# Kernel optimization log

Measured on AMD Instinct MI355X. Metric: run time of the kernel, lower is better.

## Reference

```python
import jax, jax.numpy as jnp
import numpy as np

H = 512      # hidden_size
V = 50257    # output_size (vocab)
M = 200      # memory_size
B = 64       # batch


def setup_inputs() -> dict:
    key = jax.random.key(0)
    ks = jax.random.split(key, 24)
    s = 1.0 / np.sqrt(H)
    f32 = jnp.float32
    return {
        "rmn_hidden": jax.random.normal(ks[0], (1, B, H), f32),
        "cell": jax.random.normal(ks[1], (1, B, H), f32),
        "context": jax.random.normal(ks[2], (1, B, H), f32),
        # embedding tables
        "emb": jax.random.normal(ks[3], (V, H), f32) * 0.02,
        "m_emb": jax.random.normal(ks[4], (V, H), f32) * 0.02,
        "c_emb": jax.random.normal(ks[5], (V, H), f32) * 0.02,
        # LSTMCell(2H -> H), torch gate order i, f, g, o
        "lstm_W_ih": jax.random.normal(ks[6], (4 * H, 2 * H), f32) * s,
        "lstm_W_hh": jax.random.normal(ks[7], (4 * H, H), f32) * s,
        "lstm_b_ih": jax.random.normal(ks[8], (4 * H,), f32) * s,
        "lstm_b_hh": jax.random.normal(ks[9], (4 * H,), f32) * s,
        # GRUCell(H -> H), torch gate order r, z, n
        "gru_W_ih": jax.random.normal(ks[10], (3 * H, H), f32) * s,
        "gru_W_hh": jax.random.normal(ks[11], (3 * H, H), f32) * s,
        "gru_b_ih": jax.random.normal(ks[12], (3 * H,), f32) * s,
        "gru_b_hh": jax.random.normal(ks[13], (3 * H,), f32) * s,
        # mb_attn_linear(M -> M)
        "attn_W": jax.random.normal(ks[14], (M, M), f32) * (1.0 / np.sqrt(M)),
        "attn_b": jax.random.normal(ks[15], (M,), f32) * (1.0 / np.sqrt(M)),
        # out Linear(2H -> V)
        "out_W": jax.random.normal(ks[16], (V, 2 * H), f32) * (1.0 / np.sqrt(2 * H)),
        "out_b": jax.random.normal(ks[17], (V,), f32) * (1.0 / np.sqrt(2 * H)),
        # int inputs
        "input_ids": jax.random.randint(ks[18], (1, B), 0, V, jnp.int32),
        "memory_tensor": jax.random.randint(ks[19], (M, B), 0, V, jnp.int32),
        "batch_size": B,
        "memory_size": M,
    }


def reference(rmn_hidden, cell, context, emb, m_emb, c_emb,
              lstm_W_ih, lstm_W_hh, lstm_b_ih, lstm_b_hh,
              gru_W_ih, gru_W_hh, gru_b_ih, gru_b_hh,
              attn_W, attn_b, out_W, out_b,
              input_ids, memory_tensor, batch_size, memory_size):
    sig = jax.nn.sigmoid
    h = rmn_hidden.shape[-1]
    # embedding + relu, concat with context along feature dim
    x = jax.nn.relu(emb[input_ids])                       # (1, B, H)
    ctx = context.reshape(1, batch_size, h)               # (1, B, H)
    xc = jnp.concatenate([x, ctx], axis=2)[0]             # (B, 2H)
    h0, c0 = rmn_hidden[0], cell[0]                       # (B, H)
    # LSTMCell
    gates = xc @ lstm_W_ih.T + lstm_b_ih + h0 @ lstm_W_hh.T + lstm_b_hh
    i, f, g, o = jnp.split(gates, 4, axis=-1)
    c1 = sig(f) * c0 + sig(i) * jnp.tanh(g)
    h1 = sig(o) * jnp.tanh(c1)                            # lstm_hidden (B, H)
    # memory attention
    in_mem = m_emb[memory_tensor]                         # (M, B, H)
    out_mem = c_emb[memory_tensor]                        # (M, B, H)
    attn = jnp.einsum('mbh,bh->bm', in_mem, h1)           # (B, M)
    attn = attn @ attn_W.T + attn_b
    # NOTE: original applies nn.LogSoftmax here (not Softmax) -- faithful.
    attn_dist = jax.nn.log_softmax(attn, axis=-1)         # (B, M)
    memory_context = jnp.einsum('mbh,bm->bh', out_mem, attn_dist)  # (B, H)
    # GRUCell(memory_context, h1)
    gi = memory_context @ gru_W_ih.T + gru_b_ih
    gh = h1 @ gru_W_hh.T + gru_b_hh
    gi_r, gi_z, gi_n = jnp.split(gi, 3, axis=-1)
    gh_r, gh_z, gh_n = jnp.split(gh, 3, axis=-1)
    r = sig(gi_r + gh_r)
    z = sig(gi_z + gh_z)
    n = jnp.tanh(gi_n + r * gh_n)
    mb = (1.0 - z) * n + z * h1                           # (B, H)
    # output projection + log-softmax
    mbc = jnp.concatenate([mb[None], ctx], axis=2)[0]     # (B, 2H)
    output = jax.nn.log_softmax(mbc @ out_W.T + out_b, axis=-1)  # (B, V)
    return (output, h1, c1[None])
```

## Files before the change

kernel.cpp:

```cpp
#include <hip/hip_runtime.h>
#include <math.h>

#define B 64
#define H 512
#define V 50257
#define M 200
#define H2 1024
#define H3 1536
#define H4 2048
#define NB 786

typedef short short8 __attribute__((ext_vector_type(8)));
typedef float f32x4 __attribute__((ext_vector_type(4)));

__device__ __forceinline__ float sigf(float x) { return 1.f / (1.f + expf(-x)); }

__device__ __forceinline__ short bf16c(float f) {
  unsigned u = __builtin_bit_cast(unsigned, f);
  unsigned r = u + 0x7fffu + ((u >> 16) & 1u);
  return (short)(r >> 16);
}

__global__ __launch_bounds__(256) void k_build_A(
    const float* __restrict__ emb, const float* __restrict__ ctx,
    const float* __restrict__ h0, const int* __restrict__ ids,
    short* __restrict__ A) {
  int k = blockIdx.x * 256 + threadIdx.x;
  int b = blockIdx.y;
  float v;
  if (k < 512) {
    v = emb[(size_t)ids[b] * H + k];
    v = v > 0.f ? v : 0.f;
  } else if (k < 1024) {
    v = ctx[b * H + (k - 512)];
  } else {
    v = h0[b * H + (k - 1024)];
  }
  A[b * H3 + k] = bf16c(v);
}

__global__ __launch_bounds__(256) void k_lstm_gates_mfma(
    const short* __restrict__ A, const float* __restrict__ W_ih,
    const float* __restrict__ W_hh, const float* __restrict__ b_ih,
    const float* __restrict__ b_hh, float* __restrict__ gates) {
  __shared__ float sred[3][64][16];
  const int tid = threadIdx.x;
  const int lane = tid & 63, wid = tid >> 6;
  const int col = lane & 15, g = lane >> 4;
  const int j = blockIdx.x * 16 + col;
  const int kbase = wid * 384;

  f32x4 acc[4];
  #pragma unroll
  for (int t = 0; t < 4; ++t) acc[t] = (f32x4)(0.f);

  #pragma unroll 2
  for (int it = 0; it < 12; ++it) {
    int k0 = kbase + it * 32;
    const float* wp;
    if (k0 < 1024) wp = W_ih + (size_t)j * H2 + k0 + g * 8;
    else           wp = W_hh + (size_t)j * H + (k0 - 1024) + g * 8;
    float4 wa = *(const float4*)wp;
    float4 wb = *(const float4*)(wp + 4);
    short8 bf;
    bf[0] = bf16c(wa.x); bf[1] = bf16c(wa.y); bf[2] = bf16c(wa.z); bf[3] = bf16c(wa.w);
    bf[4] = bf16c(wb.x); bf[5] = bf16c(wb.y); bf[6] = bf16c(wb.z); bf[7] = bf16c(wb.w);
    #pragma unroll
    for (int t = 0; t < 4; ++t) {
      short8 af = *(const short8*)(A + (size_t)(col + t * 16) * H3 + k0 + g * 8);
      acc[t] = __builtin_amdgcn_mfma_f32_16x16x32_bf16(af, bf, acc[t], 0, 0, 0);
    }
  }

  if (wid) {
    #pragma unroll
    for (int t = 0; t < 4; ++t)
      #pragma unroll
      for (int r = 0; r < 4; ++r) sred[wid - 1][lane][t * 4 + r] = acc[t][r];
  }
  __syncthreads();
  if (wid == 0) {
    float bias = b_ih[j] + b_hh[j];
    #pragma unroll
    for (int t = 0; t < 4; ++t)
      #pragma unroll
      for (int r = 0; r < 4; ++r) {
        float s = acc[t][r] + sred[0][lane][t * 4 + r] + sred[1][lane][t * 4 + r] +
                  sred[2][lane][t * 4 + r];
        int brow = t * 16 + g * 4 + r;
        gates[brow * H4 + j] = s + bias;
      }
  }
}

__global__ __launch_bounds__(256) void k_lstm_cell(
    const float* __restrict__ gates, const float* __restrict__ c0,
    float* __restrict__ h1, float* __restrict__ c1, short* __restrict__ h1bf) {
  int idx = blockIdx.x * 256 + threadIdx.x;
  int b = idx >> 9, h = idx & 511;
  const float* g = gates + b * H4;
  float gi = g[h], gf = g[H + h], gg = g[2 * H + h], go = g[3 * H + h];
  float c = sigf(gf) * c0[idx] + sigf(gi) * tanhf(gg);
  c1[idx] = c;
  float hv = sigf(go) * tanhf(c);
  h1[idx] = hv;
  h1bf[idx] = bf16c(hv);
}

__global__ __launch_bounds__(256) void k_attn_scores(
    const float* __restrict__ m_emb, const int* __restrict__ mt,
    const float* __restrict__ h1, float* __restrict__ attn) {
  int wave = (blockIdx.x * 256 + threadIdx.x) >> 6;
  int lane = threadIdx.x & 63;
  int m = wave >> 6, b = wave & 63;
  int row = mt[m * B + b];
  const float4* e = (const float4*)(m_emb + (size_t)row * H);
  const float4* hv = (const float4*)(h1 + b * H);
  float4 a0 = e[lane], a1 = e[64 + lane];
  float4 b0 = hv[lane], b1 = hv[64 + lane];
  float acc = a0.x * b0.x + a0.y * b0.y + a0.z * b0.z + a0.w * b0.w +
              a1.x * b1.x + a1.y * b1.y + a1.z * b1.z + a1.w * b1.w;
  for (int off = 32; off > 0; off >>= 1) acc += __shfl_down(acc, off);
  if (lane == 0) attn[b * M + m] = acc;
}

__global__ __launch_bounds__(256) void k_attn_lin_lsm(
    const float* __restrict__ attn, const float* __restrict__ attn_W,
    const float* __restrict__ attn_b, float* __restrict__ attn_d) {
  __shared__ float arow[M];
  __shared__ float vals[256];
  __shared__ float red[256];
  int b = blockIdx.x, tid = threadIdx.x;
  if (tid < M) arow[tid] = attn[b * M + tid];
  __syncthreads();
  float v = -1e30f;
  if (tid < M) {
    const float* w = attn_W + tid * M;
    float a0 = attn_b[tid], a1 = 0.f;
    for (int m = 0; m < M; m += 2) {
      a0 = fmaf(arow[m], w[m], a0);
      a1 = fmaf(arow[m + 1], w[m + 1], a1);
    }
    v = a0 + a1;
  }
  vals[tid] = v;
  red[tid] = v;
  __syncthreads();
  for (int off = 128; off > 0; off >>= 1) {
    if (tid < off) red[tid] = fmaxf(red[tid], red[tid + off]);
    __syncthreads();
  }
  float mx = red[0];
  __syncthreads();
  red[tid] = (tid < M) ? expf(vals[tid] - mx) : 0.f;
  __syncthreads();
  for (int off = 128; off > 0; off >>= 1) {
    if (tid < off) red[tid] += red[tid + off];
    __syncthreads();
  }
  float lse = mx + logf(red[0]);
  if (tid < M) attn_d[b * M + tid] = vals[tid] - lse;
}

__global__ __launch_bounds__(256) void k_mem_ctx_partial(
    const float* __restrict__ c_emb, const int* __restrict__ mt,
    const float* __restrict__ attn_d, float* __restrict__ mcp) {
  int b = blockIdx.x;
  int chunk = blockIdx.y;
  int tid = threadIdx.x;
  __shared__ int rows[50];
  __shared__ float w[50];
  if (tid < 50) {
    int m = chunk * 50 + tid;
    rows[tid] = mt[m * B + b];
    w[tid] = attn_d[b * M + m];
  }
  __syncthreads();
  float acc0 = 0.f, acc1 = 0.f;
  #pragma unroll 5
  for (int i = 0; i < 50; ++i) {
    const float* e = c_emb + (size_t)rows[i] * H;
    acc0 = fmaf(w[i], e[tid], acc0);
    acc1 = fmaf(w[i], e[256 + tid], acc1);
  }
  mcp[(chunk * B + b) * H + tid] = acc0;
  mcp[(chunk * B + b) * H + 256 + tid] = acc1;
}

__global__ __launch_bounds__(256) void k_mem_ctx_reduce(
    const float* __restrict__ mcp, short* __restrict__ mcbf) {
  int idx = blockIdx.x * 256 + threadIdx.x;
  float s = 0.f;
  for (int c = 0; c < 4; ++c) s += mcp[c * (B * H) + idx];
  mcbf[idx] = bf16c(s);
}

__global__ __launch_bounds__(256) void k_gru_gates_mfma(
    const short* __restrict__ mcbf, const short* __restrict__ h1bf,
    const float* __restrict__ W_ih, const float* __restrict__ W_hh,
    const float* __restrict__ b_ih, const float* __restrict__ b_hh,
    float* __restrict__ gi, float* __restrict__ gh) {
  __shared__ float sred[3][64][16];
  const int tid = threadIdx.x;
  const int lane = tid & 63, wid = tid >> 6;
  const int col = lane & 15, g = lane >> 4;
  const int half = blockIdx.x / 96;
  const int j = (blockIdx.x % 96) * 16 + col;
  const short* A = half ? h1bf : mcbf;
  const float* W = half ? W_hh : W_ih;
  const float* bias = half ? b_hh : b_ih;
  float* out = half ? gh : gi;
  const int kbase = wid * 128;

  f32x4 acc[4];
  #pragma unroll
  for (int t = 0; t < 4; ++t) acc[t] = (f32x4)(0.f);

  #pragma unroll
  for (int it = 0; it < 4; ++it) {
    int k0 = kbase + it * 32;
    const float* wp = W + (size_t)j * H + k0 + g * 8;
    float4 wa = *(const float4*)wp;
    float4 wb = *(const float4*)(wp + 4);
    short8 bf;
    bf[0] = bf16c(wa.x); bf[1] = bf16c(wa.y); bf[2] = bf16c(wa.z); bf[3] = bf16c(wa.w);
    bf[4] = bf16c(wb.x); bf[5] = bf16c(wb.y); bf[6] = bf16c(wb.z); bf[7] = bf16c(wb.w);
    #pragma unroll
    for (int t = 0; t < 4; ++t) {
      short8 af = *(const short8*)(A + (size_t)(col + t * 16) * H + k0 + g * 8);
      acc[t] = __builtin_amdgcn_mfma_f32_16x16x32_bf16(af, bf, acc[t], 0, 0, 0);
    }
  }

  if (wid) {
    #pragma unroll
    for (int t = 0; t < 4; ++t)
      #pragma unroll
      for (int r = 0; r < 4; ++r) sred[wid - 1][lane][t * 4 + r] = acc[t][r];
  }
  __syncthreads();
  if (wid == 0) {
    float bv = bias[j];
    #pragma unroll
    for (int t = 0; t < 4; ++t)
      #pragma unroll
      for (int r = 0; r < 4; ++r) {
        float s = acc[t][r] + sred[0][lane][t * 4 + r] + sred[1][lane][t * 4 + r] +
                  sred[2][lane][t * 4 + r];
        int brow = t * 16 + g * 4 + r;
        out[brow * H3 + j] = s + bv;
      }
  }
}

__global__ __launch_bounds__(256) void k_gru_combine(
    const float* __restrict__ gi, const float* __restrict__ gh,
    const float* __restrict__ h1, const float* __restrict__ ctx,
    short* __restrict__ Abf) {
  int idx = blockIdx.x * 256 + threadIdx.x;
  int b = idx >> 9, h = idx & 511;
  const float* gib = gi + b * H3;
  const float* ghb = gh + b * H3;
  float r = sigf(gib[h] + ghb[h]);
  float z = sigf(gib[H + h] + ghb[H + h]);
  float n = tanhf(gib[2 * H + h] + r * ghb[2 * H + h]);
  float mb = (1.f - z) * n + z * h1[idx];
  Abf[b * H2 + h] = bf16c(mb);
  Abf[b * H2 + H + h] = bf16c(ctx[idx]);
}

__global__ __launch_bounds__(512) void k_out_gemm_mfma(
    const short* __restrict__ Abf, const float* __restrict__ W,
    const float* __restrict__ bias, float* __restrict__ out,
    float* __restrict__ pm, float* __restrict__ ps) {
  __shared__ short8 Wl[1024];
  __shared__ short8 Al[1024];
  __shared__ float spm[8][32];
  __shared__ float sps[8][32];
  const int tid = threadIdx.x;
  const int v0 = blockIdx.x * 64;

  const int sr = tid >> 3, sj = tid & 7;
  const int sidx = sr * 8 + (sj ^ (sr & 7));
  int vr = v0 + sr; if (vr >= V) vr = V - 1;
  const float* wsrc = W + (size_t)vr * H2 + sj * 8;
  const short8* asrc = (const short8*)(Abf + sr * H2 + sj * 8);

  const int lane = tid & 63, wid = tid >> 6;
  const int col = lane & 15, g = lane >> 4;
  const int ct = wid & 3, bh = wid >> 2;
  const int wrow = ct * 16 + col;
  const int a0r = bh * 32 + col;
  const int a1r = a0r + 16;

  f32x4 acc0 = (f32x4)(0.f), acc1 = (f32x4)(0.f);

  {
    float4 wa = *(const float4*)(wsrc);
    float4 wb = *(const float4*)(wsrc + 4);
    short8 av = asrc[0];
    short8 wv;
    wv[0] = bf16c(wa.x); wv[1] = bf16c(wa.y); wv[2] = bf16c(wa.z); wv[3] = bf16c(wa.w);
    wv[4] = bf16c(wb.x); wv[5] = bf16c(wb.y); wv[6] = bf16c(wb.z); wv[7] = bf16c(wb.w);
    Wl[sidx] = wv;
    Al[sidx] = av;
  }
  __syncthreads();

  int cur = 0;
  for (int kt = 0; kt < 16; ++kt) {
    float4 nwa, nwb;
    short8 nav;
    if (kt < 15) {
      nwa = *(const float4*)(wsrc + (kt + 1) * 64);
      nwb = *(const float4*)(wsrc + (kt + 1) * 64 + 4);
      nav = asrc[(kt + 1) * 8];
    }
    const short8* Wb = Wl + cur * 512;
    const short8* Ab = Al + cur * 512;
    #pragma unroll
    for (int kw = 0; kw < 2; ++kw) {
      int c = kw * 4 + g;
      short8 bf  = Wb[wrow * 8 + (c ^ (wrow & 7))];
      short8 af0 = Ab[a0r * 8 + (c ^ (a0r & 7))];
      short8 af1 = Ab[a1r * 8 + (c ^ (a1r & 7))];
      acc0 = __builtin_amdgcn_mfma_f32_16x16x32_bf16(af0, bf, acc0, 0, 0, 0);
      acc1 = __builtin_amdgcn_mfma_f32_16x16x32_bf16(af1, bf, acc1, 0, 0, 0);
    }
    if (kt < 15) {
      short8 wv;
      wv[0] = bf16c(nwa.x); wv[1] = bf16c(nwa.y); wv[2] = bf16c(nwa.z); wv[3] = bf16c(nwa.w);
      wv[4] = bf16c(nwb.x); wv[5] = bf16c(nwb.y); wv[6] = bf16c(nwb.z); wv[7] = bf16c(nwb.w);
      Wl[(cur ^ 1) * 512 + sidx] = wv;
      Al[(cur ^ 1) * 512 + sidx] = nav;
      __syncthreads();
      cur ^= 1;
    }
  }

  const int v = v0 + ct * 16 + col;
  const float bv = (v < V) ? bias[v] : 0.f;
  #pragma unroll
  for (int ai = 0; ai < 2; ++ai) {
    f32x4 a = ai ? acc1 : acc0;
    #pragma unroll
    for (int r = 0; r < 4; ++r) {
      int b = bh * 32 + ai * 16 + g * 4 + r;
      float x = a[r] + bv;
      if (v < V) out[(size_t)b * V + v] = x;
      float xm = (v < V) ? x : -1e30f;
      float mx = xm;
      #pragma unroll
      for (int off = 1; off < 16; off <<= 1) mx = fmaxf(mx, __shfl_xor(mx, off));
      float e = (v < V) ? expf(xm - mx) : 0.f;
      #pragma unroll
      for (int off = 1; off < 16; off <<= 1) e += __shfl_xor(e, off);
      if (col == 0) {
        spm[wid][ai * 16 + g * 4 + r] = mx;
        sps[wid][ai * 16 + g * 4 + r] = e;
      }
    }
  }
  __syncthreads();
  if (tid < 64) {
    int b = tid;
    int wbase = (b >> 5) * 4;
    int bl = b & 31;
    float m = spm[wbase][bl], s = sps[wbase][bl];
    #pragma unroll
    for (int w = 1; w < 4; ++w) {
      float m2 = spm[wbase + w][bl], s2 = sps[wbase + w][bl];
      float nm = fmaxf(m, m2);
      s = s * expf(m - nm) + s2 * expf(m2 - nm);
      m = nm;
    }
    pm[(size_t)b * NB + blockIdx.x] = m;
    ps[(size_t)b * NB + blockIdx.x] = s;
  }
}

__global__ __launch_bounds__(256) void k_lsm_finalize(
    const float* __restrict__ pm, const float* __restrict__ ps,
    float* __restrict__ lse) {
  int b = blockIdx.x, tid = threadIdx.x;
  float m = -1e30f, s = 0.f;
  for (int gq = tid; gq < NB; gq += 256) {
    float m2 = pm[(size_t)b * NB + gq], s2 = ps[(size_t)b * NB + gq];
    float nm = fmaxf(m, m2);
    s = s * expf(m - nm) + s2 * expf(m2 - nm);
    m = nm;
  }
  __shared__ float sm[256], ss[256];
  sm[tid] = m; ss[tid] = s;
  __syncthreads();
  for (int off = 128; off > 0; off >>= 1) {
    if (tid < off) {
      float m1 = sm[tid], s1 = ss[tid];
      float m2 = sm[tid + off], s2 = ss[tid + off];
      float nm = fmaxf(m1, m2);
      sm[tid] = nm;
      ss[tid] = s1 * expf(m1 - nm) + s2 * expf(m2 - nm);
    }
    __syncthreads();
  }
  if (tid == 0) lse[b] = sm[0] + logf(ss[0]);
}

__global__ __launch_bounds__(256) void k_lsm_apply(
    float* __restrict__ out, const float* __restrict__ lse) {
  int b = blockIdx.y, tid = threadIdx.x;
  float l = lse[b];
  int v = blockIdx.x * 1024 + tid * 4;
  float* row = out + (size_t)b * V;
  if (v + 3 < V) {
    float4 x = *(const float4*)(row + v);
    x.x -= l; x.y -= l; x.z -= l; x.w -= l;
    *(float4*)(row + v) = x;
  } else {
    for (int i = 0; i < 4 && v + i < V; ++i) row[v + i] -= l;
  }
}

extern "C" void kernel_launch(void* const* d_in, const int* in_sizes, int n_in,
                              void* d_out, int out_size, void* d_ws, size_t ws_size,
                              hipStream_t stream) {
  const float* h0    = (const float*)d_in[0];
  const float* c0    = (const float*)d_in[1];
  const float* ctx   = (const float*)d_in[2];
  const float* emb   = (const float*)d_in[3];
  const float* m_emb = (const float*)d_in[4];
  const float* c_emb = (const float*)d_in[5];
  const float* lWih  = (const float*)d_in[6];
  const float* lWhh  = (const float*)d_in[7];
  const float* lbih  = (const float*)d_in[8];
  const float* lbhh  = (const float*)d_in[9];
  const float* gWih  = (const float*)d_in[10];
  const float* gWhh  = (const float*)d_in[11];
  const float* gbih  = (const float*)d_in[12];
  const float* gbhh  = (const float*)d_in[13];
  const float* aW    = (const float*)d_in[14];
  const float* ab    = (const float*)d_in[15];
  const float* oW    = (const float*)d_in[16];
  const float* ob    = (const float*)d_in[17];
  const int* ids     = (const int*)d_in[18];
  const int* mt      = (const int*)d_in[19];

  float* out = (float*)d_out;
  float* h1  = out + (size_t)B * V;
  float* c1  = h1 + B * H;

  float* ws    = (float*)d_ws;
  short* Albf  = (short*)ws;
  float* gates = ws + 49152;
  short* h1bf  = (short*)(gates + B * H4);
  float* attn  = gates + B * H4 + 16384;
  float* attnd = attn + B * M;
  float* mcp   = attnd + B * M;
  short* mcbf  = (short*)(mcp + 4 * B * H);
  float* gi    = mcp + 4 * B * H + 16384;
  float* gh    = gi + B * H3;
  short* Abf   = (short*)(gh + B * H3);
  float* pm    = gh + B * H3 + 32768;
  float* ps    = pm + (size_t)B * NB;
  float* lse   = ps + (size_t)B * NB;

  dim3 g1(6, B);
  k_build_A<<<g1, 256, 0, stream>>>(emb, ctx, h0, ids, Albf);
  k_lstm_gates_mfma<<<128, 256, 0, stream>>>(Albf, lWih, lWhh, lbih, lbhh, gates);
  k_lstm_cell<<<(B * H) / 256, 256, 0, stream>>>(gates, c0, h1, c1, h1bf);
  k_attn_scores<<<(M * B) / 4, 256, 0, stream>>>(m_emb, mt, h1, attn);
  k_attn_lin_lsm<<<B, 256, 0, stream>>>(attn, aW, ab, attnd);
  dim3 g6(B, 4);
  k_mem_ctx_partial<<<g6, 256, 0, stream>>>(c_emb, mt, attnd, mcp);
  k_mem_ctx_reduce<<<(B * H) / 256, 256, 0, stream>>>(mcp, mcbf);
  k_gru_gates_mfma<<<192, 256, 0, stream>>>(mcbf, h1bf, gWih, gWhh, gbih, gbhh, gi, gh);
  k_gru_combine<<<(B * H) / 256, 256, 0, stream>>>(gi, gh, h1, ctx, Abf);
  k_out_gemm_mfma<<<NB, 512, 0, stream>>>(Abf, oW, ob, out, pm, ps);
  k_lsm_finalize<<<B, 256, 0, stream>>>(pm, ps, lse);
  dim3 g11(50, B);
  k_lsm_apply<<<g11, 256, 0, stream>>>(out, lse);
}
```

Before: 110.7 us.

## Restructure output GEMM staging into four wide K-stages with direct A loads

Rewrites the output projection kernel's main loop. It now stages 256-wide K chunks of W (8 rows per wave, coalesced float4 per lane) into a swizzled double-buffered LDS tile over four stages, instead of sixteen 64-wide stages. The activation operand is read directly from global/L2 instead of through LDS. This cuts the number of barriers and gives each lane more loads in flight, at the cost of more registers and of the loads no longer overlapping compute, since each next stage is loaded after the current one finishes. Conversion helpers are also factored out in the other GEMMs.

```diff
diff --git a/kernel.cpp b/kernel.cpp
--- a/kernel.cpp
+++ b/kernel.cpp
@@ -11,6 +11,7 @@
 #define NB 786
 
 typedef short short8 __attribute__((ext_vector_type(8)));
+typedef short short4v __attribute__((ext_vector_type(4)));
 typedef float f32x4 __attribute__((ext_vector_type(4)));
 
 __device__ __forceinline__ float sigf(float x) { return 1.f / (1.f + expf(-x)); }
@@ -19,6 +20,19 @@
   unsigned u = __builtin_bit_cast(unsigned, f);
   unsigned r = u + 0x7fffu + ((u >> 16) & 1u);
   return (short)(r >> 16);
+}
+
+__device__ __forceinline__ short8 cvt8(float4 a, float4 b) {
+  short8 w;
+  w[0] = bf16c(a.x); w[1] = bf16c(a.y); w[2] = bf16c(a.z); w[3] = bf16c(a.w);
+  w[4] = bf16c(b.x); w[5] = bf16c(b.y); w[6] = bf16c(b.z); w[7] = bf16c(b.w);
+  return w;
+}
+
+__device__ __forceinline__ short4v cvt4(float4 a) {
+  short4v w;
+  w[0] = bf16c(a.x); w[1] = bf16c(a.y); w[2] = bf16c(a.z); w[3] = bf16c(a.w);
+  return w;
 }
 
 __global__ __launch_bounds__(256) void k_build_A(
@@ -62,9 +76,7 @@
     else           wp = W_hh + (size_t)j * H + (k0 - 1024) + g * 8;
     float4 wa = *(const float4*)wp;
     float4 wb = *(const float4*)(wp + 4);
-    short8 bf;
-    bf[0] = bf16c(wa.x); bf[1] = bf16c(wa.y); bf[2] = bf16c(wa.z); bf[3] = bf16c(wa.w);
-    bf[4] = bf16c(wb.x); bf[5] = bf16c(wb.y); bf[6] = bf16c(wb.z); bf[7] = bf16c(wb.w);
+    short8 bf = cvt8(wa, wb);
     #pragma unroll
     for (int t = 0; t < 4; ++t) {
       short8 af = *(const short8*)(A + (size_t)(col + t * 16) * H3 + k0 + g * 8);
@@ -222,9 +234,7 @@
     const float* wp = W + (size_t)j * H + k0 + g * 8;
     float4 wa = *(const float4*)wp;
     float4 wb = *(const float4*)(wp + 4);
-    short8 bf;
-    bf[0] = bf16c(wa.x); bf[1] = bf16c(wa.y); bf[2] = bf16c(wa.z); bf[3] = bf16c(wa.w);
-    bf[4] = bf16c(wb.x); bf[5] = bf16c(wb.y); bf[6] = bf16c(wb.z); bf[7] = bf16c(wb.w);
+    short8 bf = cvt8(wa, wb);
     #pragma unroll
     for (int t = 0; t < 4; ++t) {
       short8 af = *(const short8*)(A + (size_t)(col + t * 16) * H + k0 + g * 8);
@@ -273,70 +283,75 @@
     const short* __restrict__ Abf, const float* __restrict__ W,
     const float* __restrict__ bias, float* __restrict__ out,
     float* __restrict__ pm, float* __restrict__ ps) {
-  __shared__ short8 Wl[1024];
-  __shared__ short8 Al[1024];
+  __shared__ short4v Wl[2][4096];
   __shared__ float spm[8][32];
   __shared__ float sps[8][32];
   const int tid = threadIdx.x;
+  const int lane = tid & 63, wid = tid >> 6;
   const int v0 = blockIdx.x * 64;
 
-  const int sr = tid >> 3, sj = tid & 7;
-  const int sidx = sr * 8 + (sj ^ (sr & 7));
-  int vr = v0 + sr; if (vr >= V) vr = V - 1;
-  const float* wsrc = W + (size_t)vr * H2 + sj * 8;
-  const short8* asrc = (const short8*)(Abf + sr * H2 + sj * 8);
-
-  const int lane = tid & 63, wid = tid >> 6;
+  const float* wsrc[8];
+  #pragma unroll
+  for (int r = 0; r < 8; ++r) {
+    int vr = v0 + wid * 8 + r;
+    if (vr >= V) vr = V - 1;
+    wsrc[r] = W + (size_t)vr * H2 + lane * 4;
+  }
+  const int swrow = wid * 8;
+  const int wr_c = lane >> 1;
+  const int wr_h = lane & 1;
+
   const int col = lane & 15, g = lane >> 4;
   const int ct = wid & 3, bh = wid >> 2;
   const int wrow = ct * 16 + col;
-  const int a0r = bh * 32 + col;
-  const int a1r = a0r + 16;
+  const short* a0p = Abf + (size_t)(bh * 32 + col) * H2;
+  const short* a1p = a0p + (size_t)16 * H2;
 
   f32x4 acc0 = (f32x4)(0.f), acc1 = (f32x4)(0.f);
-
-  {
-    float4 wa = *(const float4*)(wsrc);
-    float4 wb = *(const float4*)(wsrc + 4);
-    short8 av = asrc[0];
-    short8 wv;
-    wv[0] = bf16c(wa.x); wv[1] = bf16c(wa.y); wv[2] = bf16c(wa.z); wv[3] = bf16c(wa.w);
-    wv[4] = bf16c(wb.x); wv[5] = bf16c(wb.y); wv[6] = bf16c(wb.z); wv[7] = bf16c(wb.w);
-    Wl[sidx] = wv;
-    Al[sidx] = av;
-  }
-  __syncthreads();
-
-  int cur = 0;
-  for (int kt = 0; kt < 16; ++kt) {
-    float4 nwa, nwb;
-    short8 nav;
-    if (kt < 15) {
-      nwa = *(const float4*)(wsrc + (kt + 1) * 64);
-      nwb = *(const float4*)(wsrc + (kt + 1) * 64 + 4);
-      nav = asrc[(kt + 1) * 8];
-    }
-    const short8* Wb = Wl + cur * 512;
-    const short8* Ab = Al + cur * 512;
-    #pragma unroll
-    for (int kw = 0; kw < 2; ++kw) {
-      int c = kw * 4 + g;
-      short8 bf  = Wb[wrow * 8 + (c ^ (wrow & 7))];
-      short8 af0 = Ab[a0r * 8 + (c ^ (a0r & 7))];
-      short8 af1 = Ab[a1r * 8 + (c ^ (a1r & 7))];
-      acc0 = __builtin_amdgcn_mfma_f32_16x16x32_bf16(af0, bf, acc0, 0, 0, 0);
-      acc1 = __builtin_amdgcn_mfma_f32_16x16x32_bf16(af1, bf, acc1, 0, 0, 0);
-    }
-    if (kt < 15) {
-      short8 wv;
-      wv[0] = bf16c(nwa.x); wv[1] = bf16c(nwa.y); wv[2] = bf16c(nwa.z); wv[3] = bf16c(nwa.w);
-      wv[4] = bf16c(nwb.x); wv[5] = bf16c(nwb.y); wv[6] = bf16c(nwb.z); wv[7] = bf16c(nwb.w);
-      Wl[(cur ^ 1) * 512 + sidx] = wv;
-      Al[(cur ^ 1) * 512 + sidx] = nav;
-      __syncthreads();
-      cur ^= 1;
-    }
-  }
+  float4 wreg[8];
+
+#define STAGE_LOAD(s)                                                        \
+  { _Pragma("unroll") for (int r = 0; r < 8; ++r)                            \
+      wreg[r] = *(const float4*)(wsrc[r] + (s) * 256); }
+
+#define STAGE_WRITE(bufi)                                                    \
+  { _Pragma("unroll") for (int r = 0; r < 8; ++r) {                          \
+      int slot = (swrow + r) * 64 + (wr_c ^ r) * 2 + wr_h;                   \
+      Wl[bufi][slot] = cvt4(wreg[r]); } }
+
+#define COMPUTE(bufi, s)                                                     \
+  { _Pragma("unroll") for (int ks = 0; ks < 4; ++ks) {                       \
+      _Pragma("unroll") for (int kw = 0; kw < 2; ++kw) {                     \
+        int c = ks * 8 + kw * 4 + g;                                         \
+        short8 bf = *(const short8*)&Wl[bufi][wrow * 64 + (c ^ (wrow & 7)) * 2]; \
+        int kg = (s) * 256 + ks * 64 + kw * 32 + g * 8;                      \
+        short8 af0 = *(const short8*)(a0p + kg);                             \
+        short8 af1 = *(const short8*)(a1p + kg);                             \
+        acc0 = __builtin_amdgcn_mfma_f32_16x16x32_bf16(af0, bf, acc0, 0, 0, 0); \
+        acc1 = __builtin_amdgcn_mfma_f32_16x16x32_bf16(af1, bf, acc1, 0, 0, 0); \
+      } } }
+
+  STAGE_LOAD(0);
+  STAGE_WRITE(0);
+  __syncthreads();
+
+  COMPUTE(0, 0);
+  STAGE_LOAD(1);
+  STAGE_WRITE(1);
+  __syncthreads();
+  COMPUTE(1, 1);
+  STAGE_LOAD(2);
+  STAGE_WRITE(0);
+  __syncthreads();
+  COMPUTE(0, 2);
+  STAGE_LOAD(3);
+  STAGE_WRITE(1);
+  __syncthreads();
+  COMPUTE(1, 3);
+
+#undef STAGE_LOAD
+#undef STAGE_WRITE
+#undef COMPUTE
 
   const int v = v0 + ct * 16 + col;
   const float bv = (v < V) ? bias[v] : 0.f;
```

After: 146.9 us. 32.6% more time.

## Stage full W tile in LDS once; stream A fragments from global

Applied to the files above, without the earlier changes.

The output GEMM kernel now loads the entire 64x1024 weight tile into LDS (128 KB as bf16) in one burst, with each thread issuing many wide loads, behind a single barrier. This replaces the 16-step double-buffered loop that synchronized every k-step. The A operand is now read straight from global or L2 into registers with a one-step prefetch, and it no longer goes through LDS. The goal is to raise memory-level parallelism on the weight stream and cut barriers. The cost is much lower occupancy, since 128 KB of LDS per block allows about one block per CU, and there is no overlap between the load phase and the MFMA phase.

```diff
diff --git a/kernel.cpp b/kernel.cpp
--- a/kernel.cpp
+++ b/kernel.cpp
@@ -19,6 +19,13 @@
   unsigned u = __builtin_bit_cast(unsigned, f);
   unsigned r = u + 0x7fffu + ((u >> 16) & 1u);
   return (short)(r >> 16);
+}
+
+__device__ __forceinline__ short8 cvt8(float4 a, float4 b) {
+  short8 w;
+  w[0] = bf16c(a.x); w[1] = bf16c(a.y); w[2] = bf16c(a.z); w[3] = bf16c(a.w);
+  w[4] = bf16c(b.x); w[5] = bf16c(b.y); w[6] = bf16c(b.z); w[7] = bf16c(b.w);
+  return w;
 }
 
 __global__ __launch_bounds__(256) void k_build_A(
@@ -62,9 +69,7 @@
     else           wp = W_hh + (size_t)j * H + (k0 - 1024) + g * 8;
     float4 wa = *(const float4*)wp;
     float4 wb = *(const float4*)(wp + 4);
-    short8 bf;
-    bf[0] = bf16c(wa.x); bf[1] = bf16c(wa.y); bf[2] = bf16c(wa.z); bf[3] = bf16c(wa.w);
-    bf[4] = bf16c(wb.x); bf[5] = bf16c(wb.y); bf[6] = bf16c(wb.z); bf[7] = bf16c(wb.w);
+    short8 bf = cvt8(wa, wb);
     #pragma unroll
     for (int t = 0; t < 4; ++t) {
       short8 af = *(const short8*)(A + (size_t)(col + t * 16) * H3 + k0 + g * 8);
@@ -222,9 +227,7 @@
     const float* wp = W + (size_t)j * H + k0 + g * 8;
     float4 wa = *(const float4*)wp;
     float4 wb = *(const float4*)(wp + 4);
-    short8 bf;
-    bf[0] = bf16c(wa.x); bf[1] = bf16c(wa.y); bf[2] = bf16c(wa.z); bf[3] = bf16c(wa.w);
-    bf[4] = bf16c(wb.x); bf[5] = bf16c(wb.y); bf[6] = bf16c(wb.z); bf[7] = bf16c(wb.w);
+    short8 bf = cvt8(wa, wb);
     #pragma unroll
     for (int t = 0; t < 4; ++t) {
       short8 af = *(const short8*)(A + (size_t)(col + t * 16) * H + k0 + g * 8);
@@ -273,70 +276,55 @@
     const short* __restrict__ Abf, const float* __restrict__ W,
     const float* __restrict__ bias, float* __restrict__ out,
     float* __restrict__ pm, float* __restrict__ ps) {
-  __shared__ short8 Wl[1024];
-  __shared__ short8 Al[1024];
-  __shared__ float spm[8][32];
-  __shared__ float sps[8][32];
+  __shared__ short8 Wl[8192];
   const int tid = threadIdx.x;
+  const int lane = tid & 63, wid = tid >> 6;
   const int v0 = blockIdx.x * 64;
 
-  const int sr = tid >> 3, sj = tid & 7;
-  const int sidx = sr * 8 + (sj ^ (sr & 7));
-  int vr = v0 + sr; if (vr >= V) vr = V - 1;
-  const float* wsrc = W + (size_t)vr * H2 + sj * 8;
-  const short8* asrc = (const short8*)(Abf + sr * H2 + sj * 8);
-
-  const int lane = tid & 63, wid = tid >> 6;
+  {
+    const int sr = tid >> 3, seg = tid & 7;
+    int vr = v0 + sr; if (vr >= V) vr = V - 1;
+    const float* wsrc = W + (size_t)vr * H2 + seg * 128;
+    const int sbase = sr * 128;
+    const int sxor = sr & 7;
+    #pragma unroll
+    for (int rd = 0; rd < 8; ++rd) {
+      float4 f0 = *(const float4*)(wsrc + rd * 16);
+      float4 f1 = *(const float4*)(wsrc + rd * 16 + 4);
+      float4 f2 = *(const float4*)(wsrc + rd * 16 + 8);
+      float4 f3 = *(const float4*)(wsrc + rd * 16 + 12);
+      int c0 = seg * 16 + rd * 2;
+      Wl[sbase + (c0 ^ sxor)]       = cvt8(f0, f1);
+      Wl[sbase + ((c0 + 1) ^ sxor)] = cvt8(f2, f3);
+    }
+  }
+  __syncthreads();
+
   const int col = lane & 15, g = lane >> 4;
   const int ct = wid & 3, bh = wid >> 2;
   const int wrow = ct * 16 + col;
-  const int a0r = bh * 32 + col;
-  const int a1r = a0r + 16;
+  const int wbase = wrow * 128, wx = wrow & 7;
+  const short* a0p = Abf + (size_t)(bh * 32 + col) * H2;
+  const short* a1p = a0p + 16 * H2;
 
   f32x4 acc0 = (f32x4)(0.f), acc1 = (f32x4)(0.f);
-
-  {
-    float4 wa = *(const float4*)(wsrc);
-    float4 wb = *(const float4*)(wsrc + 4);
-    short8 av = asrc[0];
-    short8 wv;
-    wv[0] = bf16c(wa.x); wv[1] = bf16c(wa.y); wv[2] = bf16c(wa.z); wv[3] = bf16c(wa.w);
-    wv[4] = bf16c(wb.x); wv[5] = bf16c(wb.y); wv[6] = bf16c(wb.z); wv[7] = bf16c(wb.w);
-    Wl[sidx] = wv;
-    Al[sidx] = av;
-  }
-  __syncthreads();
-
-  int cur = 0;
-  for (int kt = 0; kt < 16; ++kt) {
-    float4 nwa, nwb;
-    short8 nav;
-    if (kt < 15) {
-      nwa = *(const float4*)(wsrc + (kt + 1) * 64);
-      nwb = *(const float4*)(wsrc + (kt + 1) * 64 + 4);
-      nav = asrc[(kt + 1) * 8];
-    }
-    const short8* Wb = Wl + cur * 512;
-    const short8* Ab = Al + cur * 512;
-    #pragma unroll
-    for (int kw = 0; kw < 2; ++kw) {
-      int c = kw * 4 + g;
-      short8 bf  = Wb[wrow * 8 + (c ^ (wrow & 7))];
-      short8 af0 = Ab[a0r * 8 + (c ^ (a0r & 7))];
-      short8 af1 = Ab[a1r * 8 + (c ^ (a1r & 7))];
-      acc0 = __builtin_amdgcn_mfma_f32_16x16x32_bf16(af0, bf, acc0, 0, 0, 0);
-      acc1 = __builtin_amdgcn_mfma_f32_16x16x32_bf16(af1, bf, acc1, 0, 0, 0);
-    }
-    if (kt < 15) {
-      short8 wv;
-      wv[0] = bf16c(nwa.x); wv[1] = bf16c(nwa.y); wv[2] = bf16c(nwa.z); wv[3] = bf16c(nwa.w);
-      wv[4] = bf16c(nwb.x); wv[5] = bf16c(nwb.y); wv[6] = bf16c(nwb.z); wv[7] = bf16c(nwb.w);
-      Wl[(cur ^ 1) * 512 + sidx] = wv;
-      Al[(cur ^ 1) * 512 + sidx] = nav;
-      __syncthreads();
-      cur ^= 1;
-    }
-  }
+  short8 af0 = *(const short8*)(a0p + g * 8);
+  short8 af1 = *(const short8*)(a1p + g * 8);
+  #pragma unroll
+  for (int ks = 0; ks < 32; ++ks) {
+    short8 bf = Wl[wbase + ((ks * 4 + g) ^ wx)];
+    short8 ca = af0, cb = af1;
+    if (ks < 31) {
+      af0 = *(const short8*)(a0p + (ks + 1) * 32 + g * 8);
+      af1 = *(const short8*)(a1p + (ks + 1) * 32 + g * 8);
+    }
+    acc0 = __builtin_amdgcn_mfma_f32_16x16x32_bf16(ca, bf, acc0, 0, 0, 0);
+    acc1 = __builtin_amdgcn_mfma_f32_16x16x32_bf16(cb, bf, acc1, 0, 0, 0);
+  }
+
+  __syncthreads();
+  float* spm = (float*)Wl;
+  float* sps = spm + 256;
 
   const int v = v0 + ct * 16 + col;
   const float bv = (v < V) ? bias[v] : 0.f;
@@ -356,20 +344,20 @@
       #pragma unroll
       for (int off = 1; off < 16; off <<= 1) e += __shfl_xor(e, off);
       if (col == 0) {
-        spm[wid][ai * 16 + g * 4 + r] = mx;
-        sps[wid][ai * 16 + g * 4 + r] = e;
+        spm[wid * 32 + ai * 16 + g * 4 + r] = mx;
+        sps[wid * 32 + ai * 16 + g * 4 + r] = e;
       }
     }
   }
   __syncthreads();
   if (tid < 64) {
     int b = tid;
-    int wbase = (b >> 5) * 4;
+    int wbase2 = (b >> 5) * 4;
     int bl = b & 31;
-    float m = spm[wbase][bl], s = sps[wbase][bl];
+    float m = spm[wbase2 * 32 + bl], s = sps[wbase2 * 32 + bl];
     #pragma unroll
     for (int w = 1; w < 4; ++w) {
-      float m2 = spm[wbase + w][bl], s2 = sps[wbase + w][bl];
+      float m2 = spm[(wbase2 + w) * 32 + bl], s2 = sps[(wbase2 + w) * 32 + bl];
       float nm = fmaxf(m, m2);
       s = s * expf(m - nm) + s2 * expf(m2 - nm);
       m = nm;
```

Result: slower. 185.6 us (+67.6%).

## Halve output GEMM tile to 32 vocab rows and read activations from global

Applied to the files above, without the earlier changes.

The output projection kernel now uses 32 vocab rows per block with 256 threads, giving about twice as many blocks (1571) to spread over the compute units. The activation operand is no longer staged in LDS. Each wave reads it straight from global memory and relies on cache hits, because the 64x1024 bf16 activation matrix is small and shared by all blocks. This cuts LDS use and traffic per block and may raise occupancy, but it adds repeated global or L2 reads of the activations and doubles the number of partial log-softmax entries the finalize step must combine.

```diff
diff --git a/kernel.cpp b/kernel.cpp
--- a/kernel.cpp
+++ b/kernel.cpp
@@ -8,7 +8,7 @@
 #define H2 1024
 #define H3 1536
 #define H4 2048
-#define NB 786
+#define NB2 1571
 
 typedef short short8 __attribute__((ext_vector_type(8)));
 typedef float f32x4 __attribute__((ext_vector_type(4)));
@@ -19,6 +19,13 @@
   unsigned u = __builtin_bit_cast(unsigned, f);
   unsigned r = u + 0x7fffu + ((u >> 16) & 1u);
   return (short)(r >> 16);
+}
+
+__device__ __forceinline__ short8 cvt8(float4 a, float4 b) {
+  short8 w;
+  w[0] = bf16c(a.x); w[1] = bf16c(a.y); w[2] = bf16c(a.z); w[3] = bf16c(a.w);
+  w[4] = bf16c(b.x); w[5] = bf16c(b.y); w[6] = bf16c(b.z); w[7] = bf16c(b.w);
+  return w;
 }
 
 __global__ __launch_bounds__(256) void k_build_A(
@@ -62,9 +69,7 @@
     else           wp = W_hh + (size_t)j * H + (k0 - 1024) + g * 8;
     float4 wa = *(const float4*)wp;
     float4 wb = *(const float4*)(wp + 4);
-    short8 bf;
-    bf[0] = bf16c(wa.x); bf[1] = bf16c(wa.y); bf[2] = bf16c(wa.z); bf[3] = bf16c(wa.w);
-    bf[4] = bf16c(wb.x); bf[5] = bf16c(wb.y); bf[6] = bf16c(wb.z); bf[7] = bf16c(wb.w);
+    short8 bf = cvt8(wa, wb);
     #pragma unroll
     for (int t = 0; t < 4; ++t) {
       short8 af = *(const short8*)(A + (size_t)(col + t * 16) * H3 + k0 + g * 8);
@@ -222,9 +227,7 @@
     const float* wp = W + (size_t)j * H + k0 + g * 8;
     float4 wa = *(const float4*)wp;
     float4 wb = *(const float4*)(wp + 4);
-    short8 bf;
-    bf[0] = bf16c(wa.x); bf[1] = bf16c(wa.y); bf[2] = bf16c(wa.z); bf[3] = bf16c(wa.w);
-    bf[4] = bf16c(wb.x); bf[5] = bf16c(wb.y); bf[6] = bf16c(wb.z); bf[7] = bf16c(wb.w);
+    short8 bf = cvt8(wa, wb);
     #pragma unroll
     for (int t = 0; t < 4; ++t) {
       short8 af = *(const short8*)(A + (size_t)(col + t * 16) * H + k0 + g * 8);
@@ -269,70 +272,58 @@
   Abf[b * H2 + H + h] = bf16c(ctx[idx]);
 }
 
-__global__ __launch_bounds__(512) void k_out_gemm_mfma(
+__global__ __launch_bounds__(256) void k_out_gemm_mfma(
     const short* __restrict__ Abf, const float* __restrict__ W,
     const float* __restrict__ bias, float* __restrict__ out,
     float* __restrict__ pm, float* __restrict__ ps) {
-  __shared__ short8 Wl[1024];
-  __shared__ short8 Al[1024];
-  __shared__ float spm[8][32];
-  __shared__ float sps[8][32];
+  __shared__ short8 Wl[512];
+  __shared__ float spm[4][32];
+  __shared__ float sps[4][32];
   const int tid = threadIdx.x;
-  const int v0 = blockIdx.x * 64;
+  const int lane = tid & 63, wid = tid >> 6;
+  const int v0 = blockIdx.x * 32;
 
   const int sr = tid >> 3, sj = tid & 7;
   const int sidx = sr * 8 + (sj ^ (sr & 7));
   int vr = v0 + sr; if (vr >= V) vr = V - 1;
   const float* wsrc = W + (size_t)vr * H2 + sj * 8;
-  const short8* asrc = (const short8*)(Abf + sr * H2 + sj * 8);
-
-  const int lane = tid & 63, wid = tid >> 6;
+
   const int col = lane & 15, g = lane >> 4;
-  const int ct = wid & 3, bh = wid >> 2;
+  const int ct = wid & 1, bh = wid >> 1;
   const int wrow = ct * 16 + col;
-  const int a0r = bh * 32 + col;
-  const int a1r = a0r + 16;
+  const short* a0p = Abf + (size_t)(bh * 32 + col) * H2 + g * 8;
+  const short* a1p = a0p + 16 * H2;
 
   f32x4 acc0 = (f32x4)(0.f), acc1 = (f32x4)(0.f);
 
   {
     float4 wa = *(const float4*)(wsrc);
     float4 wb = *(const float4*)(wsrc + 4);
-    short8 av = asrc[0];
-    short8 wv;
-    wv[0] = bf16c(wa.x); wv[1] = bf16c(wa.y); wv[2] = bf16c(wa.z); wv[3] = bf16c(wa.w);
-    wv[4] = bf16c(wb.x); wv[5] = bf16c(wb.y); wv[6] = bf16c(wb.z); wv[7] = bf16c(wb.w);
-    Wl[sidx] = wv;
-    Al[sidx] = av;
+    Wl[sidx] = cvt8(wa, wb);
   }
   __syncthreads();
 
   int cur = 0;
   for (int kt = 0; kt < 16; ++kt) {
     float4 nwa, nwb;
-    short8 nav;
     if (kt < 15) {
       nwa = *(const float4*)(wsrc + (kt + 1) * 64);
       nwb = *(const float4*)(wsrc + (kt + 1) * 64 + 4);
-      nav = asrc[(kt + 1) * 8];
-    }
-    const short8* Wb = Wl + cur * 512;
-    const short8* Ab = Al + cur * 512;
-    #pragma unroll
-    for (int kw = 0; kw < 2; ++kw) {
-      int c = kw * 4 + g;
-      short8 bf  = Wb[wrow * 8 + (c ^ (wrow & 7))];
-      short8 af0 = Ab[a0r * 8 + (c ^ (a0r & 7))];
-      short8 af1 = Ab[a1r * 8 + (c ^ (a1r & 7))];
-      acc0 = __builtin_amdgcn_mfma_f32_16x16x32_bf16(af0, bf, acc0, 0, 0, 0);
-      acc1 = __builtin_amdgcn_mfma_f32_16x16x32_bf16(af1, bf, acc1, 0, 0, 0);
+    }
+    {
+      const short8* Wb = Wl + cur * 256;
+      #pragma unroll
+      for (int kw = 0; kw < 2; ++kw) {
+        int c = kw * 4 + g;
+        short8 bf  = Wb[wrow * 8 + (c ^ (wrow & 7))];
+        short8 af0 = *(const short8*)(a0p + kt * 64 + kw * 32);
+        short8 af1 = *(const short8*)(a1p + kt * 64 + kw * 32);
+        acc0 = __builtin_amdgcn_mfma_f32_16x16x32_bf16(af0, bf, acc0, 0, 0, 0);
+        acc1 = __builtin_amdgcn_mfma_f32_16x16x32_bf16(af1, bf, acc1, 0, 0, 0);
+      }
     }
     if (kt < 15) {
-      short8 wv;
-      wv[0] = bf16c(nwa.x); wv[1] = bf16c(nwa.y); wv[2] = bf16c(nwa.z); wv[3] = bf16c(nwa.w);
-      wv[4] = bf16c(nwb.x); wv[5] = bf16c(nwb.y); wv[6] = bf16c(nwb.z); wv[7] = bf16c(nwb.w);
-      Wl[(cur ^ 1) * 512 + sidx] = wv;
-      Al[(cur ^ 1) * 512 + sidx] = nav;
+      Wl[(cur ^ 1) * 256 + sidx] = cvt8(nwa, nwb);
       __syncthreads();
       cur ^= 1;
     }
@@ -364,18 +355,14 @@
   __syncthreads();
   if (tid < 64) {
     int b = tid;
-    int wbase = (b >> 5) * 4;
+    int w0 = (b >> 5) * 2;
     int bl = b & 31;
-    float m = spm[wbase][bl], s = sps[wbase][bl];
-    #pragma unroll
-    for (int w = 1; w < 4; ++w) {
-      float m2 = spm[wbase + w][bl], s2 = sps[wbase + w][bl];
-      float nm = fmaxf(m, m2);
-      s = s * expf(m - nm) + s2 * expf(m2 - nm);
-      m = nm;
-    }
-    pm[(size_t)b * NB + blockIdx.x] = m;
-    ps[(size_t)b * NB + blockIdx.x] = s;
+    float m1 = spm[w0][bl],     s1 = sps[w0][bl];
+    float m2 = spm[w0 + 1][bl], s2 = sps[w0 + 1][bl];
+    float nm = fmaxf(m1, m2);
+    float s = s1 * expf(m1 - nm) + s2 * expf(m2 - nm);
+    pm[(size_t)b * NB2 + blockIdx.x] = nm;
+    ps[(size_t)b * NB2 + blockIdx.x] = s;
   }
 }
 
@@ -384,8 +371,8 @@
     float* __restrict__ lse) {
   int b = blockIdx.x, tid = threadIdx.x;
   float m = -1e30f, s = 0.f;
-  for (int gq = tid; gq < NB; gq += 256) {
-    float m2 = pm[(size_t)b * NB + gq], s2 = ps[(size_t)b * NB + gq];
+  for (int gq = tid; gq < NB2; gq += 256) {
+    float m2 = pm[(size_t)b * NB2 + gq], s2 = ps[(size_t)b * NB2 + gq];
     float nm = fmaxf(m, m2);
     s = s * expf(m - nm) + s2 * expf(m2 - nm);
     m = nm;
@@ -461,8 +448,8 @@
   float* gh    = gi + B * H3;
   short* Abf   = (short*)(gh + B * H3);
   float* pm    = gh + B * H3 + 32768;
-  float* ps    = pm + (size_t)B * NB;
-  float* lse   = ps + (size_t)B * NB;
+  float* ps    = pm + (size_t)B * NB2;
+  float* lse   = ps + (size_t)B * NB2;
 
   dim3 g1(6, B);
   k_build_A<<<g1, 256, 0, stream>>>(emb, ctx, h0, ids, Albf);
@@ -475,7 +462,7 @@
   k_mem_ctx_reduce<<<(B * H) / 256, 256, 0, stream>>>(mcp, mcbf);
   k_gru_gates_mfma<<<192, 256, 0, stream>>>(mcbf, h1bf, gWih, gWhh, gbih, gbhh, gi, gh);
   k_gru_combine<<<(B * H) / 256, 256, 0, stream>>>(gi, gh, h1, ctx, Abf);
-  k_out_gemm_mfma<<<NB, 512, 0, stream>>>(Abf, oW, ob, out, pm, ps);
+  k_out_gemm_mfma<<<NB2, 256, 0, stream>>>(Abf, oW, ob, out, pm, ps);
   k_lsm_finalize<<<B, 256, 0, stream>>>(pm, ps, lse);
   dim3 g11(50, B);
   k_lsm_apply<<<g11, 256, 0, stream>>>(out, lse);
```

New measurement: 137.3 us. +24.0%, slower.
